# Kernel optimization log

Measured on AMD Instinct MI355X. Metric: run time of the kernel, lower is better.

The kernel has to match this reference:

```python
import jax, jax.numpy as jnp
import numpy as np

E4M3_MAX = 448.0


def fp8_qdq(x):
    """Per-tensor fp8 (e4m3) quantize-dequantize with amax scaling."""
    amax = jnp.max(jnp.abs(x))
    scale = jnp.maximum(amax / E4M3_MAX, 1e-12).astype(x.dtype)
    q = (x / scale).astype(jnp.float8_e4m3fn).astype(x.dtype)
    return q * scale


def setup_inputs() -> dict:
    key = jax.random.key(0)
    k1, k2, k3 = jax.random.split(key, 3)
    A, B, C, D, E = 4, 512, 512, 32, 128
    inputs = jax.random.normal(k1, (A, B, C), dtype=jnp.float32)
    kernel1 = jax.random.normal(k2, (C, D, E), dtype=jnp.float32) * 0.02
    kernel2 = jax.random.normal(k3, (C, D, E), dtype=jnp.float32) * 0.02
    return {"inputs": inputs, "kernel1": kernel1, "kernel2": kernel2}


def reference(inputs, kernel1, kernel2):
    # Layer 1: EinsumDenseFp8('abc,cde->abde')
    x_q = fp8_qdq(inputs)
    w1_q = fp8_qdq(kernel1)
    h = jnp.einsum('abc,cde->abde', x_q, w1_q)  # (A,B,D,E)
    # Layer 2: EinsumDenseFp8('abde,cde->abce', is_last=True)
    h_q = fp8_qdq(h)
    w2_q = fp8_qdq(kernel2)
    out = jnp.einsum('abde,cde->abce', h_q, w2_q)  # (A,B,C,E)
    return out
```

## Files before the change

kernel.cpp:

```cpp
#include <hip/hip_runtime.h>

typedef float f32x4 __attribute__((ext_vector_type(4)));

#define AX_X 0
#define AX_W1 1
#define AX_W2 2

__device__ __forceinline__ unsigned char fp8_encode(float t) {
  unsigned tb = __float_as_uint(t);
  unsigned sgn = (tb >> 24) & 0x80u;
  float a = fabsf(t);
  unsigned sb = (unsigned)(int)rintf(a * 512.0f);
  unsigned u = tb & 0x7fffffffu;
  unsigned rem = u & 0xFFFFFu;
  unsigned keep = u & ~0xFFFFFu;
  unsigned inc = (rem > 0x80000u || (rem == 0x80000u && (keep & 0x100000u))) ? 0x100000u : 0u;
  keep += inc;
  int e = (int)(keep >> 23) - 127;
  unsigned nb = (unsigned)((e + 7) << 3) | ((keep >> 20) & 7u);
  unsigned b = (a < 0.015625f) ? sb : nb;
  return (unsigned char)(b | sgn);
}

__device__ __forceinline__ float scale_from(const float* __restrict__ part, int which) {
  float m = 0.f;
#pragma unroll
  for (int i = 0; i < 64; i++) m = fmaxf(m, part[which * 64 + i]);
  return fmaxf(m / 448.0f, 1e-12f);
}

__device__ __forceinline__ float scale_raw(float rawmax) {
  return fmaxf(rawmax / 448.0f, 1e-12f);
}

__device__ __forceinline__ void gll16(const void* g, void* l) {
  __builtin_amdgcn_global_load_lds(
      (const __attribute__((address_space(1))) unsigned int*)g,
      (__attribute__((address_space(3))) unsigned int*)l, 16, 0, 0);
}

__global__ __launch_bounds__(256, 4) void k_amax3(const float* __restrict__ x,
                                                  const float* __restrict__ w1,
                                                  const float* __restrict__ w2,
                                                  float* __restrict__ part) {
  __shared__ float wmax[4];
  int which = blockIdx.y;
  const float* p = which == 0 ? x : (which == 1 ? w1 : w2);
  int n4 = which == 0 ? (1048576 / 4) : (2097152 / 4);
  float m = 0.f;
  for (int i = blockIdx.x * 256 + threadIdx.x; i < n4; i += gridDim.x * 256) {
    float4 v = ((const float4*)p)[i];
    m = fmaxf(m, fmaxf(fmaxf(fabsf(v.x), fabsf(v.y)), fmaxf(fabsf(v.z), fabsf(v.w))));
  }
  for (int off = 32; off; off >>= 1) m = fmaxf(m, __shfl_xor(m, off));
  int t = threadIdx.x;
  if ((t & 63) == 0) wmax[t >> 6] = m;
  __syncthreads();
  if (t == 0)
    part[which * 64 + blockIdx.x] =
        fmaxf(fmaxf(wmax[0], wmax[1]), fmaxf(wmax[2], wmax[3]));
}

__global__ __launch_bounds__(256, 2) void k_quant_all(const float* __restrict__ x,
                                                      const float* __restrict__ w1,
                                                      const float* __restrict__ w2,
                                                      unsigned char* __restrict__ qx,
                                                      unsigned char* __restrict__ qw1t,
                                                      unsigned char* __restrict__ qw2,
                                                      const float* __restrict__ part) {
  __shared__ float tile[64 * 68];
  int b = blockIdx.x, t = threadIdx.x;
  if (b < 256) {
    float s = scale_from(part, AX_X);
    int i = b * 256 + t;
    const float4* src = (const float4*)x + (size_t)i * 4;
    union { unsigned char bb[16]; uint4 u; } o;
#pragma unroll
    for (int p = 0; p < 4; p++) {
      float4 v = src[p];
      o.bb[p * 4 + 0] = fp8_encode(v.x / s);
      o.bb[p * 4 + 1] = fp8_encode(v.y / s);
      o.bb[p * 4 + 2] = fp8_encode(v.z / s);
      o.bb[p * 4 + 3] = fp8_encode(v.w / s);
    }
    *(uint4*)(qx + (size_t)i * 16) = o.u;
  } else if (b < 768) {
    float s = scale_from(part, AX_W1);
    int idx = b - 256;
    int n0 = (idx & 63) * 64, c0 = (idx >> 6) * 64;
    int row = t >> 2, q4 = t & 3;
    const float* src = w1 + (size_t)(c0 + row) * 4096 + n0 + q4 * 16;
#pragma unroll
    for (int p = 0; p < 4; p++) {
      float4 v = *(const float4*)(src + p * 4);
      *(float4*)&tile[row * 68 + q4 * 16 + p * 4] = v;
    }
    __syncthreads();
    int nl = t >> 2, ch = t & 3;
    union { unsigned char bb[16]; uint4 u; } o;
#pragma unroll
    for (int j = 0; j < 16; j++) o.bb[j] = fp8_encode(tile[(ch * 16 + j) * 68 + nl] / s);
    *(uint4*)(qw1t + (size_t)(n0 + nl) * 512 + c0 + ch * 16) = o.u;
  } else {
    float s = scale_from(part, AX_W2);
    int row = b - 768;
    const float* sp = w2 + (size_t)row * 4096;
#pragma unroll
    for (int p = 0; p < 4; p++) {
      int n = (p * 256 + t) * 4;
      float4 v = *(const float4*)(sp + n);
      *(float4*)&tile[(n >> 7) * 132 + (n & 127)] = v;
    }
    __syncthreads();
    int e = t >> 1, half = t & 1;
    union { unsigned char bb[16]; uint4 u; } o;
#pragma unroll
    for (int j = 0; j < 16; j++) o.bb[j] = fp8_encode(tile[(half * 16 + j) * 132 + e] / s);
    *(uint4*)(qw2 + ((size_t)e * 512 + row) * 32 + half * 16) = o.u;
  }
}

__global__ __launch_bounds__(256, 2) void k_quant_h(const float* __restrict__ src,
                                                    unsigned char* __restrict__ dst,
                                                    const float* __restrict__ hpart) {
  __shared__ float tile[32 * 132];
  int row = blockIdx.x, t = threadIdx.x;
  float2 hv = ((const float2*)hpart)[t];
  float m = fmaxf(hv.x, hv.y);
  for (int off = 32; off; off >>= 1) m = fmaxf(m, __shfl_xor(m, off));
  if ((t & 63) == 0) tile[t >> 6] = m;
  __syncthreads();
  float s = scale_raw(fmaxf(fmaxf(tile[0], tile[1]), fmaxf(tile[2], tile[3])));
  __syncthreads();
  const float* sp = src + (size_t)row * 4096;
#pragma unroll
  for (int p = 0; p < 4; p++) {
    int n = (p * 256 + t) * 4;
    float4 v = *(const float4*)(sp + n);
    *(float4*)&tile[(n >> 7) * 132 + (n & 127)] = v;
  }
  __syncthreads();
  int e = t >> 1, half = t & 1;
  union { unsigned char b[16]; uint4 u; } o;
#pragma unroll
  for (int j = 0; j < 16; j++) o.b[j] = fp8_encode(tile[(half * 16 + j) * 132 + e] / s);
  *(uint4*)(dst + ((size_t)e * 2048 + row) * 32 + half * 16) = o.u;
}

__global__ __launch_bounds__(256, 2) void k_gemm1(const unsigned char* __restrict__ qa,
                                                  const unsigned char* __restrict__ qb,
                                                  float* __restrict__ h,
                                                  const float* __restrict__ part,
                                                  float* __restrict__ hpart) {
  __shared__ unsigned char As[16384], Bs[16384];
  __shared__ float wred[4];
  int m0 = blockIdx.y * 128, n0 = blockIdx.x * 128;
  int t = threadIdx.x, lane = t & 63, w = t >> 6, wr = w >> 1, wc = w & 1;
  f32x4 acc[4][4] = {};
  const unsigned char* ag = qa + (size_t)(m0 + (t >> 1)) * 512 + (t & 1) * 16;
  const unsigned char* bg = qb + (size_t)(n0 + (t >> 1)) * 512 + (t & 1) * 16;
  const int ldst = 16 * t;
  const int abase = (wr * 64 + (lane & 15)) * 32 + ((lane >> 4) << 3);
  const int bbase = (wc * 64 + (lane & 15)) * 32 + ((lane >> 4) << 3);

  for (int k0 = 0; k0 < 512; k0 += 128) {
#pragma unroll
    for (int j = 0; j < 4; j++) {
      gll16(ag + k0 + j * 32, As + j * 4096 + ldst);
      gll16(bg + k0 + j * 32, Bs + j * 4096 + ldst);
    }
    __syncthreads();
#pragma unroll
    for (int kk = 0; kk < 4; kk++) {
      long a[4], b[4];
#pragma unroll
      for (int i = 0; i < 4; i++) {
        a[i] = *(const long*)(As + kk * 4096 + abase + i * 512);
        b[i] = *(const long*)(Bs + kk * 4096 + bbase + i * 512);
      }
#pragma unroll
      for (int mi = 0; mi < 4; mi++)
#pragma unroll
        for (int ni = 0; ni < 4; ni++)
          acc[mi][ni] = __builtin_amdgcn_mfma_f32_16x16x32_fp8_fp8(a[mi], b[ni], acc[mi][ni], 0, 0, 0);
    }
    __syncthreads();
  }

  float s1 = scale_from(part, AX_X) * scale_from(part, AX_W1);
  float lmax = 0.f;
#pragma unroll
  for (int mi = 0; mi < 4; mi++)
#pragma unroll
    for (int ni = 0; ni < 4; ni++)
#pragma unroll
      for (int r = 0; r < 4; r++) {
        float v = acc[mi][ni][r] * s1;
        h[(size_t)(m0 + wr * 64 + mi * 16 + ((lane >> 4) << 2) + r) * 4096 +
          (n0 + wc * 64 + ni * 16 + (lane & 15))] = v;
        lmax = fmaxf(lmax, fabsf(v));
      }
  for (int off = 32; off; off >>= 1) lmax = fmaxf(lmax, __shfl_xor(lmax, off));
  if (lane == 0) wred[w] = lmax;
  __syncthreads();
  if (t == 0)
    hpart[blockIdx.y * 32 + blockIdx.x] =
        fmaxf(fmaxf(wred[0], wred[1]), fmaxf(wred[2], wred[3]));
}

__global__ __launch_bounds__(512, 2) void k_gemm2(const unsigned char* __restrict__ qh,
                                                  const unsigned char* __restrict__ qw2,
                                                  const float* __restrict__ part,
                                                  const float* __restrict__ hpart,
                                                  float* __restrict__ out) {
  __shared__ float lbuf[8 * 64 * 34];
  int bid = blockIdx.x;
  int sw = (bid & 7) * 256 + (bid >> 3);
  int m0 = (sw >> 5) * 32, c0 = (sw & 31) * 16;
  int t = threadIdx.x, lane = t & 63, w = t >> 6;
  float m = hpart[t];
  for (int off = 32; off; off >>= 1) m = fmaxf(m, __shfl_xor(m, off));
  if (lane == 0) lbuf[w] = m;
  __syncthreads();
  float hm = lbuf[0];
#pragma unroll
  for (int i = 1; i < 8; i++) hm = fmaxf(hm, lbuf[i]);
  float s2 = scale_raw(hm) * scale_from(part, AX_W2);
  __syncthreads();

  int mw = m0 + (w >> 2) * 16;
  int e0 = (w & 3) * 32;
  const unsigned char* A = qh + ((size_t)e0 * 2048 + mw + (lane & 15)) * 32 + ((lane >> 4) << 3);
  const unsigned char* B = qw2 + ((size_t)e0 * 512 + c0 + (lane & 15)) * 32 + ((lane >> 4) << 3);
  f32x4 acc[32];
#pragma unroll
  for (int e = 0; e < 32; e++) {
    long a = *(const long*)(A + (size_t)e * 2048 * 32);
    long b = *(const long*)(B + (size_t)e * 512 * 32);
    f32x4 z = {0.f, 0.f, 0.f, 0.f};
    acc[e] = __builtin_amdgcn_mfma_f32_16x16x32_fp8_fp8(a, b, z, 0, 0, 0);
  }
  float* lw = lbuf + w * (64 * 34);
#pragma unroll
  for (int r = 0; r < 4; r++) {
#pragma unroll
    for (int g = 0; g < 8; g++) {
      *(float2*)&lw[lane * 34 + 4 * g] =
          make_float2(acc[4 * g + 0][r] * s2, acc[4 * g + 1][r] * s2);
      *(float2*)&lw[lane * 34 + 4 * g + 2] =
          make_float2(acc[4 * g + 2][r] * s2, acc[4 * g + 3][r] * s2);
    }
#pragma unroll
    for (int i = 0; i < 8; i++) {
      int p = i * 8 + (lane >> 3);
      float2 u0 = *(const float2*)&lw[p * 34 + (lane & 7) * 4];
      float2 u1 = *(const float2*)&lw[p * 34 + (lane & 7) * 4 + 2];
      float* dst = out + ((size_t)(mw + ((p >> 4) << 2) + r) * 512 + c0 + (p & 15)) * 128 +
                   e0 + (lane & 7) * 4;
      f32x4 vv = {u0.x, u0.y, u1.x, u1.y};
      __builtin_nontemporal_store(vv, (f32x4*)dst);
    }
  }
}

extern "C" void kernel_launch(void* const* d_in, const int* in_sizes, int n_in,
                              void* d_out, int out_size, void* d_ws, size_t ws_size,
                              hipStream_t stream) {
  const float* x  = (const float*)d_in[0];
  const float* w1 = (const float*)d_in[1];
  const float* w2 = (const float*)d_in[2];
  float* out = (float*)d_out;

  float* part  = (float*)d_ws;
  float* hpart = (float*)d_ws + 256;
  unsigned char* base = (unsigned char*)d_ws + 4096;
  unsigned char* qx   = base;
  unsigned char* qw1t = qx   + (size_t)2048 * 512;
  unsigned char* qw2  = qw1t + (size_t)4096 * 512;
  unsigned char* qh   = qw2  + (size_t)128 * 512 * 32;
  float* h = (float*)(qh + (size_t)128 * 2048 * 32);

  k_amax3<<<dim3(64, 3), dim3(256), 0, stream>>>(x, w1, w2, part);
  k_quant_all<<<dim3(1280), dim3(256), 0, stream>>>(x, w1, w2, qx, qw1t, qw2, part);
  k_gemm1<<<dim3(32, 16), dim3(256), 0, stream>>>(qx, qw1t, h, part, hpart);
  k_quant_h<<<dim3(2048), dim3(256), 0, stream>>>(h, qh, hpart);
  k_gemm2<<<dim3(2048), dim3(512), 0, stream>>>(qh, qw2, part, hpart, out);
}
```

Measured before the change: 164.9 us.

## Shrink GEMM1 K-tile, swizzle block order, and use nontemporal stores for h

The first fp8 GEMM now stages a 32-wide K slice per iteration instead of 128. This cuts shared memory per block from 32KB to 8KB so more blocks can be resident, at the cost of four times as many barriers per K loop. The 2D grid becomes a 1D grid with a swizzled block-to-tile mapping meant to improve L2 reuse of the A and B panels. The h output is written with nontemporal stores to avoid polluting cache; the partial-max index changes to the linear block id, which is harmless because the consumer takes a max over all 512 entries.

```diff
diff --git a/kernel.cpp b/kernel.cpp
--- a/kernel.cpp
+++ b/kernel.cpp
@@ -152,38 +152,34 @@
                                                   float* __restrict__ h,
                                                   const float* __restrict__ part,
                                                   float* __restrict__ hpart) {
-  __shared__ unsigned char As[16384], Bs[16384];
+  __shared__ unsigned char As[4096], Bs[4096];
   __shared__ float wred[4];
-  int m0 = blockIdx.y * 128, n0 = blockIdx.x * 128;
+  int bid = blockIdx.x;
+  int sw = (bid & 7) * 64 + (bid >> 3);
+  int m0 = (sw & 15) * 128, n0 = (sw >> 4) * 128;
   int t = threadIdx.x, lane = t & 63, w = t >> 6, wr = w >> 1, wc = w & 1;
   f32x4 acc[4][4] = {};
   const unsigned char* ag = qa + (size_t)(m0 + (t >> 1)) * 512 + (t & 1) * 16;
   const unsigned char* bg = qb + (size_t)(n0 + (t >> 1)) * 512 + (t & 1) * 16;
-  const int ldst = 16 * t;
+  const int wbase = w * 1024;
   const int abase = (wr * 64 + (lane & 15)) * 32 + ((lane >> 4) << 3);
   const int bbase = (wc * 64 + (lane & 15)) * 32 + ((lane >> 4) << 3);
 
-  for (int k0 = 0; k0 < 512; k0 += 128) {
-#pragma unroll
-    for (int j = 0; j < 4; j++) {
-      gll16(ag + k0 + j * 32, As + j * 4096 + ldst);
-      gll16(bg + k0 + j * 32, Bs + j * 4096 + ldst);
-    }
-    __syncthreads();
-#pragma unroll
-    for (int kk = 0; kk < 4; kk++) {
-      long a[4], b[4];
-#pragma unroll
-      for (int i = 0; i < 4; i++) {
-        a[i] = *(const long*)(As + kk * 4096 + abase + i * 512);
-        b[i] = *(const long*)(Bs + kk * 4096 + bbase + i * 512);
-      }
-#pragma unroll
-      for (int mi = 0; mi < 4; mi++)
-#pragma unroll
-        for (int ni = 0; ni < 4; ni++)
-          acc[mi][ni] = __builtin_amdgcn_mfma_f32_16x16x32_fp8_fp8(a[mi], b[ni], acc[mi][ni], 0, 0, 0);
-    }
+  for (int k0 = 0; k0 < 512; k0 += 32) {
+    gll16(ag + k0, As + wbase);
+    gll16(bg + k0, Bs + wbase);
+    __syncthreads();
+    long a[4], b[4];
+#pragma unroll
+    for (int i = 0; i < 4; i++) {
+      a[i] = *(const long*)(As + abase + i * 512);
+      b[i] = *(const long*)(Bs + bbase + i * 512);
+    }
+#pragma unroll
+    for (int mi = 0; mi < 4; mi++)
+#pragma unroll
+      for (int ni = 0; ni < 4; ni++)
+        acc[mi][ni] = __builtin_amdgcn_mfma_f32_16x16x32_fp8_fp8(a[mi], b[ni], acc[mi][ni], 0, 0, 0);
     __syncthreads();
   }
 
@@ -196,16 +192,16 @@
 #pragma unroll
       for (int r = 0; r < 4; r++) {
         float v = acc[mi][ni][r] * s1;
-        h[(size_t)(m0 + wr * 64 + mi * 16 + ((lane >> 4) << 2) + r) * 4096 +
-          (n0 + wc * 64 + ni * 16 + (lane & 15))] = v;
+        __builtin_nontemporal_store(
+            v, &h[(size_t)(m0 + wr * 64 + mi * 16 + ((lane >> 4) << 2) + r) * 4096 +
+                  (n0 + wc * 64 + ni * 16 + (lane & 15))]);
         lmax = fmaxf(lmax, fabsf(v));
       }
   for (int off = 32; off; off >>= 1) lmax = fmaxf(lmax, __shfl_xor(lmax, off));
   if (lane == 0) wred[w] = lmax;
   __syncthreads();
   if (t == 0)
-    hpart[blockIdx.y * 32 + blockIdx.x] =
-        fmaxf(fmaxf(wred[0], wred[1]), fmaxf(wred[2], wred[3]));
+    hpart[bid] = fmaxf(fmaxf(wred[0], wred[1]), fmaxf(wred[2], wred[3]));
 }
 
 __global__ __launch_bounds__(512, 2) void k_gemm2(const unsigned char* __restrict__ qh,
@@ -282,7 +278,7 @@
 
   k_amax3<<<dim3(64, 3), dim3(256), 0, stream>>>(x, w1, w2, part);
   k_quant_all<<<dim3(1280), dim3(256), 0, stream>>>(x, w1, w2, qx, qw1t, qw2, part);
-  k_gemm1<<<dim3(32, 16), dim3(256), 0, stream>>>(qx, qw1t, h, part, hpart);
+  k_gemm1<<<dim3(512), dim3(256), 0, stream>>>(qx, qw1t, h, part, hpart);
   k_quant_h<<<dim3(2048), dim3(256), 0, stream>>>(h, qh, hpart);
   k_gemm2<<<dim3(2048), dim3(512), 0, stream>>>(qh, qw2, part, hpart, out);
 }
```

Result: slower. 169.8 us (+3.0%).
